# Performance work log

Measured on AMD Instinct MI355X. Metric: run time of the kernel, lower is better.

Reference implementation:

```python
import jax, jax.numpy as jnp
import numpy as np
from jax import lax

B, S, H = 20000, 1, 1
SPIN, TRAINLEN = 365, 15000
ML, SL = 2.9086, 1.898  # hard-coded PET normalization constants from source


def setup_inputs() -> dict:
    key = jax.random.key(0)
    ks = jax.random.split(key, 24)
    inp = {
        "x": jax.random.uniform(ks[0], (B, S, 2), jnp.float32),
        "y_obs": jax.random.uniform(ks[1], (B, 1), jnp.float32),
        "p_mean": jax.random.uniform(ks[2], (1,), jnp.float32),
        "p_std": jax.random.uniform(ks[3], (1,), jnp.float32),
        "epoch": 1,
        "time_lag": 0,
    }
    mat_names = ["weight_r_yom", "weight_r_yom_fp", "weight_r_yom_gw", "weight_r_ylm",
                 "weight_r_yfm", "weight_b1_yom", "weight_b1_yom_gw", "weight_b1_yom_fp",
                 "weight_b2_ylm", "theltaC"]
    vec_names = ["bias_b0_yom", "bias_b0_yom_gw", "bias_b0_yom_fp", "bias_b0_ylm"]
    for i, n in enumerate(mat_names):
        inp[n] = jax.random.uniform(ks[4 + i], (H, H), jnp.float32)
    for i, n in enumerate(vec_names):
        inp[n] = jax.random.uniform(ks[14 + i], (H,), jnp.float32)
    return inp


def _forward(x, y_obs, p_mean, p_std, weight_r_yom, weight_r_yom_fp, weight_r_yom_gw,
             weight_r_ylm, weight_r_yfm, bias_b0_yom, weight_b1_yom, bias_b0_yom_gw,
             weight_b1_yom_gw, bias_b0_yom_fp, weight_b1_yom_fp, bias_b0_ylm,
             weight_b2_ylm, theltaC, time_lag):
    relu, sig = jax.nn.relu, jax.nn.sigmoid
    tmap = jax.tree_util.tree_map
    # gate prefactors depend only on params -> hoisted out of the scan
    denom = (jnp.exp(weight_r_yom) + jnp.exp(weight_r_yom_gw) + jnp.exp(weight_r_ylm)
             + jnp.exp(weight_r_yfm) + jnp.exp(weight_r_yom_fp))
    oo1 = jnp.exp(weight_r_yom) / denom
    oogw1 = jnp.exp(weight_r_yom_gw) / denom
    oofp1 = jnp.exp(weight_r_yom_fp) / denom
    ol1 = jnp.exp(weight_r_ylm) / denom
    expC = jnp.exp(theltaC)
    mo, so = p_mean, p_std
    obsstd = jnp.std(y_obs[SPIN:TRAINLEN], ddof=1)  # torch.std is unbiased

    def gate_step(c0, u):
        u1 = u[0].reshape(1, 1)  # precip, broadcast to [1,H]
        u2 = u[1].reshape(1, 1)  # PET
        px = relu(u1 + c0 - expC)  # bypass/overflow flux
        ib = jnp.where(u1 > 0, px / jnp.where(u1 == 0, 1.0, u1), 0.0)
        z = (c0 - mo) / so
        oo = oo1 * sig(bias_b0_yom + z @ weight_b1_yom)
        oogw = oogw1 * sig(bias_b0_yom_gw + z @ weight_b1_yom_gw)
        oofp = oofp1 * sig(bias_b0_yom_fp + z @ weight_b1_yom_fp)
        ol = ol1 * sig(bias_b0_ylm + ((u2 - ML) / SL) @ weight_b2_ylm)
        olc = jnp.where(c0 > 0, ol - relu(ol - u2 / jnp.where(c0 > 0, c0, 1.0)), ol)
        f = 1.0 - oo - oofp - oogw - olc
        c1 = f * c0 + (u1 - px)  # mass-conserving state update
        outs = {"q": oo * c0, "h": oo * c0 + px, "hfp": oofp * c0, "c": c0,
                "l": ol * c0, "lc": olc * c0, "bp": px, "gw": oogw * c0,
                "ib": ib, "oo": oo, "ol": ol, "oofp": oofp, "f": f,
                "olc": olc, "oogw": oogw}
        return c1, outs

    def b_step(c0, binp):  # outer loop over 'batch' (acts as time axis)
        b, xb = binp
        c_fin, seq_outs = lax.scan(gate_step, c0, xb)  # xb: [S,2]
        outs = tmap(lambda a: a[-1], seq_outs)  # only last t survives the store
        active = b >= time_lag
        c_new = jnp.where(active, c_fin, c0)
        outs = tmap(lambda a: jnp.where(active, a, 0.0), outs)
        return c_new, outs

    nB = x.shape[0]
    c_init = jnp.zeros((1, H), x.dtype)
    _, O = lax.scan(b_step, c_init, (jnp.arange(nB), x))
    O = tmap(lambda a: a.reshape(nB, H), O)
    obs_std = jnp.where(jnp.arange(nB)[:, None] >= time_lag, obsstd, 0.0).astype(x.dtype)
    h_nout = jnp.concatenate([O["h"], obs_std], axis=1)
    return (O["h"], O["hfp"], O["c"], O["l"], O["lc"], O["bp"], O["gw"], O["ib"],
            O["oo"], O["oofp"], O["ol"], O["olc"], O["f"], O["oogw"], h_nout, obs_std)


def reference(x, y_obs, p_mean, p_std, epoch, time_lag, weight_r_yom, weight_r_yom_fp,
              weight_r_yom_gw, weight_r_ylm, weight_r_yfm, bias_b0_yom, weight_b1_yom,
              bias_b0_yom_gw, weight_b1_yom_gw, bias_b0_yom_fp, weight_b1_yom_fp,
              bias_b0_ylm, weight_b2_ylm, theltaC):
    return _forward(x, y_obs, p_mean, p_std, weight_r_yom, weight_r_yom_fp,
                    weight_r_yom_gw, weight_r_ylm, weight_r_yfm, bias_b0_yom,
                    weight_b1_yom, bias_b0_yom_gw, weight_b1_yom_gw, bias_b0_yom_fp,
                    weight_b1_yom_fp, bias_b0_ylm, weight_b2_ylm, theltaC, time_lag)
```

## Files before the change

### kernel.cpp

```cpp
#include <hip/hip_runtime.h>
#include <math.h>

#define NB 20000
#define SPIN 365
#define TRAINLEN 15000
#define ML_C 2.9086f
#define SL_C 1.898f

#define CHUNK 8
#define WSPEC 96
#define NLANES 2500
#define NSCANBLK 40

#define EX2(x) __builtin_amdgcn_exp2f(x)
#define RCP(x) __builtin_amdgcn_rcpf(x)
#define L2E 1.4426950408889634f

__device__ __forceinline__ int clampi(int j) {
  return j < 0 ? 0 : (j > NB - 1 ? NB - 1 : j);
}

__global__ __launch_bounds__(64) void fused_kernel(
    const float* __restrict__ x, const float* __restrict__ y,
    const float* __restrict__ p_mean, const float* __restrict__ p_std,
    const int* __restrict__ time_lag,
    const float* __restrict__ w_r_yom, const float* __restrict__ w_r_yom_fp,
    const float* __restrict__ w_r_yom_gw, const float* __restrict__ w_r_ylm,
    const float* __restrict__ w_r_yfm,
    const float* __restrict__ w_b1_yom, const float* __restrict__ w_b1_yom_gw,
    const float* __restrict__ w_b1_yom_fp, const float* __restrict__ w_b2_ylm,
    const float* __restrict__ theltaC,
    const float* __restrict__ b0_yom, const float* __restrict__ b0_yom_gw,
    const float* __restrict__ b0_yom_fp, const float* __restrict__ b0_ylm,
    float* __restrict__ out) {
  const int lane = threadIdx.x;
  const int tl = time_lag[0];

  if (blockIdx.x == NSCANBLK) {
    double a = 0.0, q = 0.0;
    if (lane < 3) {
      double v = (double)y[SPIN + lane];
      a += v; q += v * v;
    }
    const float4* y4 = (const float4*)(y + 368);
    for (int i = lane; i < 3658; i += 64) {
      float4 v = y4[i];
      double v0 = v.x, v1 = v.y, v2 = v.z, v3 = v.w;
      a += v0 + v1 + v2 + v3;
      q += v0 * v0 + v1 * v1 + v2 * v2 + v3 * v3;
    }
    for (int off = 32; off > 0; off >>= 1) {
      a += __shfl_xor(a, off, 64);
      q += __shfl_xor(q, off, 64);
    }
    const double n = (double)(TRAINLEN - SPIN);
    const float sd = (float)sqrt((q - a * a / n) / (n - 1.0));
    for (int i = lane; i < NB / 4; i += 64) {
      int t = 4 * i;
      float4 v;
      v.x = (t >= tl) ? sd : 0.f;
      v.y = (t + 1 >= tl) ? sd : 0.f;
      v.z = (t + 2 >= tl) ? sd : 0.f;
      v.w = (t + 3 >= tl) ? sd : 0.f;
      *(float4*)(out + 16 * NB + t) = v;
    }
    for (int t = lane; t < NB; t += 64)
      out[14 * NB + 2 * t + 1] = (t >= tl) ? sd : 0.f;
    return;
  }

  const int gid = blockIdx.x * 64 + lane;
  const int start = gid * CHUNK;
  const int begin = start - WSPEC;

  float e1 = __expf(w_r_yom[0]);
  float e2 = __expf(w_r_yom_gw[0]);
  float e3 = __expf(w_r_ylm[0]);
  float e4 = __expf(w_r_yfm[0]);
  float e5 = __expf(w_r_yom_fp[0]);
  float rd = 1.f / (e1 + e2 + e3 + e4 + e5);
  float oo1 = e1 * rd, oogw1 = e2 * rd, oofp1 = e5 * rd, ol1 = e3 * rd;
  float expC = __expf(theltaC[0]);
  float mo = p_mean[0];
  float inv_so = 1.f / p_std[0];
  float w1 = w_b1_yom[0], w1gw = w_b1_yom_gw[0], w1fp = w_b1_yom_fp[0], w2 = w_b2_ylm[0];
  float k_oo = -L2E * (w1 * inv_so);
  float d_oo = -L2E * (b0_yom[0] - mo * inv_so * w1);
  float k_gw = -L2E * (w1gw * inv_so);
  float d_gw = -L2E * (b0_yom_gw[0] - mo * inv_so * w1gw);
  float k_fp = -L2E * (w1fp * inv_so);
  float d_fp = -L2E * (b0_yom_fp[0] - mo * inv_so * w1fp);
  float k_ol = -L2E * (w2 / SL_C);
  float d_ol = -L2E * (b0_ylm[0] - (ML_C / SL_C) * w2);

  const float2* __restrict__ xv = (const float2*)x;

  float2 xb[4];
#pragma unroll
  for (int k = 0; k < 4; ++k) xb[k] = xv[clampi(begin + k)];

  float c = 0.f;
  for (int tt = 0; tt < WSPEC; tt += 4) {
#pragma unroll
    for (int k = 0; k < 4; ++k) {
      const int idx = begin + tt + k;
      float2 xc = xb[k];
      xb[k] = xv[clampi(idx + 4)];
      if (idx >= 0) {
        float u1 = xc.x, u2 = xc.y;
        float px = fmaxf(u1 + c - expC, 0.f);
        float soo = RCP(1.f + EX2(fmaf(c, k_oo, d_oo)));
        float sgw = RCP(1.f + EX2(fmaf(c, k_gw, d_gw)));
        float sfp = RCP(1.f + EX2(fmaf(c, k_fp, d_fp)));
        float sol = RCP(1.f + EX2(fmaf(u2, k_ol, d_ol)));
        float oo = oo1 * soo, oogw = oogw1 * sgw, oofp = oofp1 * sfp, ol = ol1 * sol;
        float ratio = u2 * RCP(c);
        float olc = (c > 0.f) ? (ol - fmaxf(ol - ratio, 0.f)) : ol;
        float fg = 1.f - oo - oofp - oogw - olc;
        if (idx >= tl) c = fmaf(fg, c, u1 - px);
      }
    }
  }

  float vh[8], vhfp[8], vc[8], vl[8], vlc[8], vbp[8], vgw[8];
  float vib[8], voo[8], voofp[8], vol[8], volc[8], vf[8], voogw[8];
#pragma unroll
  for (int k = 0; k < 8; ++k) {
    const int idx = start + k;
    float2 xc = xb[k & 3];
    if (k < 4) xb[k & 3] = xv[clampi(idx + 4)];
    float u1 = xc.x, u2 = xc.y;
    float px = fmaxf(u1 + c - expC, 0.f);
    float iu = (u1 > 0.f) ? RCP(u1) : 0.f;
    float ib = px * iu;
    float soo = RCP(1.f + EX2(fmaf(c, k_oo, d_oo)));
    float sgw = RCP(1.f + EX2(fmaf(c, k_gw, d_gw)));
    float sfp = RCP(1.f + EX2(fmaf(c, k_fp, d_fp)));
    float sol = RCP(1.f + EX2(fmaf(u2, k_ol, d_ol)));
    float oo = oo1 * soo, oogw = oogw1 * sgw, oofp = oofp1 * sfp, ol = ol1 * sol;
    float ratio = u2 * RCP(c);
    float olc = (c > 0.f) ? (ol - fmaxf(ol - ratio, 0.f)) : ol;
    float fg = 1.f - oo - oofp - oogw - olc;
    bool act = idx >= tl;
    float m = act ? 1.f : 0.f;
    vh[k] = m * fmaf(oo, c, px);
    vhfp[k] = m * (oofp * c);
    vc[k] = m * c;
    vl[k] = m * (ol * c);
    vlc[k] = m * (olc * c);
    vbp[k] = m * px;
    vgw[k] = m * (oogw * c);
    vib[k] = m * ib;
    voo[k] = m * oo;
    voofp[k] = m * oofp;
    vol[k] = m * ol;
    volc[k] = m * olc;
    vf[k] = m * fg;
    voogw[k] = m * oogw;
    if (act) c = fmaf(fg, c, u1 - px);
  }

  if (gid < NLANES) {
#define ST(col, v)                                                            \
  *(float4*)(out + (col) * NB + start) = make_float4(v[0], v[1], v[2], v[3]); \
  *(float4*)(out + (col) * NB + start + 4) = make_float4(v[4], v[5], v[6], v[7]);
    ST(0, vh) ST(1, vhfp) ST(2, vc) ST(3, vl) ST(4, vlc) ST(5, vbp) ST(6, vgw)
    ST(7, vib) ST(8, voo) ST(9, voofp) ST(10, vol) ST(11, volc) ST(12, vf)
    ST(13, voogw)
#undef ST
#pragma unroll
    for (int k = 0; k < 8; ++k)
      out[14 * NB + 2 * (start + k)] = vh[k];
  }
}

extern "C" void kernel_launch(void* const* d_in, const int* in_sizes, int n_in,
                              void* d_out, int out_size, void* d_ws, size_t ws_size,
                              hipStream_t stream) {
  const float* x        = (const float*)d_in[0];
  const float* y_obs    = (const float*)d_in[1];
  const float* p_mean   = (const float*)d_in[2];
  const float* p_std    = (const float*)d_in[3];
  const int* time_lag   = (const int*)d_in[5];
  const float* w_r_yom    = (const float*)d_in[6];
  const float* w_r_yom_fp = (const float*)d_in[7];
  const float* w_r_yom_gw = (const float*)d_in[8];
  const float* w_r_ylm    = (const float*)d_in[9];
  const float* w_r_yfm    = (const float*)d_in[10];
  const float* w_b1_yom   = (const float*)d_in[11];
  const float* w_b1_yom_gw= (const float*)d_in[12];
  const float* w_b1_yom_fp= (const float*)d_in[13];
  const float* w_b2_ylm   = (const float*)d_in[14];
  const float* theltaC    = (const float*)d_in[15];
  const float* b0_yom     = (const float*)d_in[16];
  const float* b0_yom_gw  = (const float*)d_in[17];
  const float* b0_yom_fp  = (const float*)d_in[18];
  const float* b0_ylm     = (const float*)d_in[19];
  float* out = (float*)d_out;
  (void)d_ws; (void)ws_size;

  fused_kernel<<<NSCANBLK + 1, 64, 0, stream>>>(
      x, y_obs, p_mean, p_std, time_lag,
      w_r_yom, w_r_yom_fp, w_r_yom_gw, w_r_ylm, w_r_yfm,
      w_b1_yom, w_b1_yom_gw, w_b1_yom_fp, w_b2_ylm,
      theltaC, b0_yom, b0_yom_gw, b0_yom_fp, b0_ylm,
      out);
}
```

Measured before the change: 120.0 us.

## Stage each block's input window in padded LDS and simplify warmup step

Each block now loads its contiguous input window once with coalesced global loads into a bank-padded shared-memory array. The warmup and output loops then read per-lane timesteps from LDS with double-buffered register prefetch, instead of issuing strided, clamped global loads per step. The warmup step is also tidied: a branchless select for the time-lag mask, fminf for olc, and a rebalanced sum for fg. The cost is a block barrier and extra LDS traffic before the serial recurrence can start.

```diff
diff --git a/kernel.cpp b/kernel.cpp
--- a/kernel.cpp
+++ b/kernel.cpp
@@ -11,14 +11,12 @@
 #define WSPEC 96
 #define NLANES 2500
 #define NSCANBLK 40
+#define WIN 608
+#define ROW 81
 
 #define EX2(x) __builtin_amdgcn_exp2f(x)
 #define RCP(x) __builtin_amdgcn_rcpf(x)
 #define L2E 1.4426950408889634f
-
-__device__ __forceinline__ int clampi(int j) {
-  return j < 0 ? 0 : (j > NB - 1 ? NB - 1 : j);
-}
 
 __global__ __launch_bounds__(64) void fused_kernel(
     const float* __restrict__ x, const float* __restrict__ y,
@@ -69,9 +67,18 @@
     return;
   }
 
-  const int gid = blockIdx.x * 64 + lane;
-  const int start = gid * CHUNK;
-  const int begin = start - WSPEC;
+  __shared__ float2 xs[8 * ROW];
+  const float2* __restrict__ xv = (const float2*)x;
+  const int wstart = blockIdx.x * (64 * CHUNK) - WSPEC;
+
+  float2 stg[10];
+#pragma unroll
+  for (int r = 0; r < 10; ++r) {
+    int i = r * 64 + lane;
+    int g = wstart + i;
+    g = g < 0 ? 0 : (g > NB - 1 ? NB - 1 : g);
+    if (r < 9 || lane < WIN - 576) stg[r] = xv[g];
+  }
 
   float e1 = __expf(w_r_yom[0]);
   float e2 = __expf(w_r_yom_gw[0]);
@@ -92,34 +99,53 @@
   float d_fp = -L2E * (b0_yom_fp[0] - mo * inv_so * w1fp);
   float k_ol = -L2E * (w2 / SL_C);
   float d_ol = -L2E * (b0_ylm[0] - (ML_C / SL_C) * w2);
-
-  const float2* __restrict__ xv = (const float2*)x;
-
-  float2 xb[4];
-#pragma unroll
-  for (int k = 0; k < 4; ++k) xb[k] = xv[clampi(begin + k)];
+  const int tl0 = tl > 0 ? tl : 0;
+
+#pragma unroll
+  for (int r = 0; r < 10; ++r) {
+    int i = r * 64 + lane;
+    if (r < 9 || lane < WIN - 576)
+      xs[(lane & 7) * ROW + (lane >> 3) + 8 * r] = stg[r];
+    (void)i;
+  }
+  __syncthreads();
+
+  const int gid = blockIdx.x * 64 + lane;
+  const int start = gid * CHUNK;
+  const int begin = start - WSPEC;
+  const float2* __restrict__ xsl = xs + lane;
 
   float c = 0.f;
-  for (int tt = 0; tt < WSPEC; tt += 4) {
-#pragma unroll
-    for (int k = 0; k < 4; ++k) {
-      const int idx = begin + tt + k;
-      float2 xc = xb[k];
-      xb[k] = xv[clampi(idx + 4)];
-      if (idx >= 0) {
-        float u1 = xc.x, u2 = xc.y;
-        float px = fmaxf(u1 + c - expC, 0.f);
-        float soo = RCP(1.f + EX2(fmaf(c, k_oo, d_oo)));
-        float sgw = RCP(1.f + EX2(fmaf(c, k_gw, d_gw)));
-        float sfp = RCP(1.f + EX2(fmaf(c, k_fp, d_fp)));
-        float sol = RCP(1.f + EX2(fmaf(u2, k_ol, d_ol)));
-        float oo = oo1 * soo, oogw = oogw1 * sgw, oofp = oofp1 * sfp, ol = ol1 * sol;
-        float ratio = u2 * RCP(c);
-        float olc = (c > 0.f) ? (ol - fmaxf(ol - ratio, 0.f)) : ol;
-        float fg = 1.f - oo - oofp - oogw - olc;
-        if (idx >= tl) c = fmaf(fg, c, u1 - px);
-      }
-    }
+
+#define WSTEP(xc, IDX)                                                \
+  {                                                                   \
+    float u1 = (xc).x, u2 = (xc).y;                                   \
+    float soo = RCP(1.f + EX2(fmaf(c, k_oo, d_oo)));                  \
+    float sgw = RCP(1.f + EX2(fmaf(c, k_gw, d_gw)));                  \
+    float sfp = RCP(1.f + EX2(fmaf(c, k_fp, d_fp)));                  \
+    float sol = RCP(1.f + EX2(fmaf(u2, k_ol, d_ol)));                 \
+    float oo = oo1 * soo, oogw = oogw1 * sgw, oofp = oofp1 * sfp;     \
+    float ol = ol1 * sol;                                             \
+    float ratio = u2 * RCP(c);                                        \
+    float olc = (c > 0.f) ? fminf(ratio, ol) : ol;                    \
+    float px = fmaxf(u1 + c - expC, 0.f);                             \
+    float fg = 1.f - ((oo + oofp) + (oogw + olc));                    \
+    float cn = fmaf(fg, c, u1 - px);                                  \
+    c = ((IDX) >= tl0) ? cn : c;                                      \
+  }
+
+  float2 xa[8], xb[8];
+#pragma unroll
+  for (int k = 0; k < 8; ++k) xa[k] = xsl[k * ROW];
+  for (int j = 0; j < 12; j += 2) {
+#pragma unroll
+    for (int k = 0; k < 8; ++k) xb[k] = xsl[k * ROW + (j + 1)];
+#pragma unroll
+    for (int k = 0; k < 8; ++k) WSTEP(xa[k], begin + j * 8 + k)
+#pragma unroll
+    for (int k = 0; k < 8; ++k) xa[k] = xsl[k * ROW + (j + 2)];
+#pragma unroll
+    for (int k = 0; k < 8; ++k) WSTEP(xb[k], begin + (j + 1) * 8 + k)
   }
 
   float vh[8], vhfp[8], vc[8], vl[8], vlc[8], vbp[8], vgw[8];
@@ -127,9 +153,7 @@
 #pragma unroll
   for (int k = 0; k < 8; ++k) {
     const int idx = start + k;
-    float2 xc = xb[k & 3];
-    if (k < 4) xb[k & 3] = xv[clampi(idx + 4)];
-    float u1 = xc.x, u2 = xc.y;
+    float u1 = xa[k].x, u2 = xa[k].y;
     float px = fmaxf(u1 + c - expC, 0.f);
     float iu = (u1 > 0.f) ? RCP(u1) : 0.f;
     float ib = px * iu;
@@ -141,7 +165,7 @@
     float ratio = u2 * RCP(c);
     float olc = (c > 0.f) ? (ol - fmaxf(ol - ratio, 0.f)) : ol;
     float fg = 1.f - oo - oofp - oogw - olc;
-    bool act = idx >= tl;
+    bool act = idx >= tl0;
     float m = act ? 1.f : 0.f;
     vh[k] = m * fmaf(oo, c, px);
     vhfp[k] = m * (oofp * c);
```

Measured after the change: 120.4 us. Within noise of the previous version (+0.4%).

## Stage input window in shared memory and halve speculative warm-up length

Applied to the files above, without the earlier changes.

Each block now loads its input window of x into shared memory with coalesced loads, using a padded layout so each lane reads its own time step conflict-free. The speculative warm-up scan that lets each lane reach a converged state is cut from 96 to 48 steps, and the output loop streams scalar stores instead of buffering values for float4 stores. The serial dependency chain on each lane becomes shorter and global load latency leaves the critical path. In exchange, the shorter warm-up risks a less accurate converged state at chunk boundaries, and the scalar stores may coalesce worse.

```diff
diff --git a/kernel.cpp b/kernel.cpp
--- a/kernel.cpp
+++ b/kernel.cpp
@@ -8,17 +8,15 @@
 #define SL_C 1.898f
 
 #define CHUNK 8
-#define WSPEC 96
+#define WSPEC 48
 #define NLANES 2500
 #define NSCANBLK 40
+#define WIN 560
+#define ROW 71
 
 #define EX2(x) __builtin_amdgcn_exp2f(x)
 #define RCP(x) __builtin_amdgcn_rcpf(x)
 #define L2E 1.4426950408889634f
-
-__device__ __forceinline__ int clampi(int j) {
-  return j < 0 ? 0 : (j > NB - 1 ? NB - 1 : j);
-}
 
 __global__ __launch_bounds__(64) void fused_kernel(
     const float* __restrict__ x, const float* __restrict__ y,
@@ -69,9 +67,17 @@
     return;
   }
 
-  const int gid = blockIdx.x * 64 + lane;
-  const int start = gid * CHUNK;
-  const int begin = start - WSPEC;
+  __shared__ float2 xs[8 * ROW];
+  const float2* __restrict__ xv = (const float2*)x;
+  const int wstart = blockIdx.x * (64 * CHUNK) - WSPEC;
+
+  float2 stg[9];
+#pragma unroll
+  for (int r = 0; r < 9; ++r) {
+    int g = wstart + r * 64 + lane;
+    g = g < 0 ? 0 : (g > NB - 1 ? NB - 1 : g);
+    if (r < 8 || lane < WIN - 512) stg[r] = xv[g];
+  }
 
   float e1 = __expf(w_r_yom[0]);
   float e2 = __expf(w_r_yom_gw[0]);
@@ -92,44 +98,49 @@
   float d_fp = -L2E * (b0_yom_fp[0] - mo * inv_so * w1fp);
   float k_ol = -L2E * (w2 / SL_C);
   float d_ol = -L2E * (b0_ylm[0] - (ML_C / SL_C) * w2);
-
-  const float2* __restrict__ xv = (const float2*)x;
-
-  float2 xb[4];
+  const int tl0 = tl > 0 ? tl : 0;
+
 #pragma unroll
-  for (int k = 0; k < 4; ++k) xb[k] = xv[clampi(begin + k)];
+  for (int r = 0; r < 9; ++r) {
+    if (r < 8 || lane < WIN - 512)
+      xs[(lane & 7) * ROW + (lane >> 3) + 8 * r] = stg[r];
+  }
+  __syncthreads();
+
+  const int gid = blockIdx.x * 64 + lane;
+  const int start = gid * CHUNK;
+  const int begin = start - WSPEC;
 
   float c = 0.f;
-  for (int tt = 0; tt < WSPEC; tt += 4) {
-#pragma unroll
-    for (int k = 0; k < 4; ++k) {
-      const int idx = begin + tt + k;
-      float2 xc = xb[k];
-      xb[k] = xv[clampi(idx + 4)];
-      if (idx >= 0) {
-        float u1 = xc.x, u2 = xc.y;
-        float px = fmaxf(u1 + c - expC, 0.f);
-        float soo = RCP(1.f + EX2(fmaf(c, k_oo, d_oo)));
-        float sgw = RCP(1.f + EX2(fmaf(c, k_gw, d_gw)));
-        float sfp = RCP(1.f + EX2(fmaf(c, k_fp, d_fp)));
-        float sol = RCP(1.f + EX2(fmaf(u2, k_ol, d_ol)));
-        float oo = oo1 * soo, oogw = oogw1 * sgw, oofp = oofp1 * sfp, ol = ol1 * sol;
-        float ratio = u2 * RCP(c);
-        float olc = (c > 0.f) ? (ol - fmaxf(ol - ratio, 0.f)) : ol;
-        float fg = 1.f - oo - oofp - oogw - olc;
-        if (idx >= tl) c = fmaf(fg, c, u1 - px);
-      }
-    }
-  }
-
-  float vh[8], vhfp[8], vc[8], vl[8], vlc[8], vbp[8], vgw[8];
-  float vib[8], voo[8], voofp[8], vol[8], volc[8], vf[8], voogw[8];
-#pragma unroll
+  float2 cur = xs[lane];
+
+#pragma unroll 1
+  for (int t = 0; t < WSPEC; ++t) {
+    const int tn = t + 1;
+    float2 nxt = xs[((tn & 7) * ROW) + lane + (tn >> 3)];
+    float u1 = cur.x, u2 = cur.y;
+    float soo = RCP(1.f + EX2(fmaf(c, k_oo, d_oo)));
+    float sgw = RCP(1.f + EX2(fmaf(c, k_gw, d_gw)));
+    float sfp = RCP(1.f + EX2(fmaf(c, k_fp, d_fp)));
+    float sol = RCP(1.f + EX2(fmaf(u2, k_ol, d_ol)));
+    float oo = oo1 * soo, oogw = oogw1 * sgw, oofp = oofp1 * sfp;
+    float ol = ol1 * sol;
+    float ratio = u2 * RCP(c);
+    float olc = (c > 0.f) ? fminf(ratio, ol) : ol;
+    float px = fmaxf(u1 + c - expC, 0.f);
+    float fg = 1.f - ((oo + oofp) + (oogw + olc));
+    float cn = fmaf(fg, c, u1 - px);
+    c = ((begin + t) >= tl0) ? cn : c;
+    cur = nxt;
+  }
+
+  const bool w = (gid < NLANES);
+  float* __restrict__ op = out + start;
+#pragma unroll 1
   for (int k = 0; k < 8; ++k) {
-    const int idx = start + k;
-    float2 xc = xb[k & 3];
-    if (k < 4) xb[k & 3] = xv[clampi(idx + 4)];
-    float u1 = xc.x, u2 = xc.y;
+    const int tn = WSPEC + k + 1;
+    float2 nxt = xs[((tn & 7) * ROW) + lane + (tn >> 3)];
+    float u1 = cur.x, u2 = cur.y;
     float px = fmaxf(u1 + c - expC, 0.f);
     float iu = (u1 > 0.f) ? RCP(u1) : 0.f;
     float ib = px * iu;
@@ -141,36 +152,28 @@
     float ratio = u2 * RCP(c);
     float olc = (c > 0.f) ? (ol - fmaxf(ol - ratio, 0.f)) : ol;
     float fg = 1.f - oo - oofp - oogw - olc;
-    bool act = idx >= tl;
+    bool act = (start + k) >= tl0;
     float m = act ? 1.f : 0.f;
-    vh[k] = m * fmaf(oo, c, px);
-    vhfp[k] = m * (oofp * c);
-    vc[k] = m * c;
-    vl[k] = m * (ol * c);
-    vlc[k] = m * (olc * c);
-    vbp[k] = m * px;
-    vgw[k] = m * (oogw * c);
-    vib[k] = m * ib;
-    voo[k] = m * oo;
-    voofp[k] = m * oofp;
-    vol[k] = m * ol;
-    volc[k] = m * olc;
-    vf[k] = m * fg;
-    voogw[k] = m * oogw;
+    float h = m * fmaf(oo, c, px);
+    if (w) {
+      op[0 * NB + k]  = h;
+      op[1 * NB + k]  = m * (oofp * c);
+      op[2 * NB + k]  = m * c;
+      op[3 * NB + k]  = m * (ol * c);
+      op[4 * NB + k]  = m * (olc * c);
+      op[5 * NB + k]  = m * px;
+      op[6 * NB + k]  = m * (oogw * c);
+      op[7 * NB + k]  = m * ib;
+      op[8 * NB + k]  = m * oo;
+      op[9 * NB + k]  = m * oofp;
+      op[10 * NB + k] = m * ol;
+      op[11 * NB + k] = m * olc;
+      op[12 * NB + k] = m * fg;
+      op[13 * NB + k] = m * oogw;
+      out[14 * NB + 2 * (start + k)] = h;
+    }
     if (act) c = fmaf(fg, c, u1 - px);
-  }
-
-  if (gid < NLANES) {
-#define ST(col, v)                                                            \
-  *(float4*)(out + (col) * NB + start) = make_float4(v[0], v[1], v[2], v[3]); \
-  *(float4*)(out + (col) * NB + start + 4) = make_float4(v[4], v[5], v[6], v[7]);
-    ST(0, vh) ST(1, vhfp) ST(2, vc) ST(3, vl) ST(4, vlc) ST(5, vbp) ST(6, vgw)
-    ST(7, vib) ST(8, voo) ST(9, voofp) ST(10, vol) ST(11, volc) ST(12, vf)
-    ST(13, voogw)
-#undef ST
-#pragma unroll
-    for (int k = 0; k < 8; ++k)
-      out[14 * NB + 2 * (start + k)] = vh[k];
+    cur = nxt;
   }
 }
 
```

Result: no change. 118.6 us (-1.1%).
